# Kernel tuning notes

Hardware: AMD Instinct MI355X
Metric: run time of the kernel (lower is better)

Reference implementation:

```python
import jax, jax.numpy as jnp
import numpy as np

G, N = 1024, 40            # graphs, nodes per graph (complete graphs)
SLOPE = 0.1                # leaky relu negative slope
SMAT_IDX = jnp.array([0, 1, 2, 3, 1, 4, 5, 6, 2, 5, 7, 8, 3, 6, 8, 9])


def setup_inputs() -> dict:
    key = jax.random.key(0)
    ks = jax.random.split(key, 24)

    # --- graph structure: G identical complete graphs of N nodes ---
    ii, jj = np.meshgrid(np.arange(N), np.arange(N), indexing="ij")
    mask = ii != jj
    src_l, dst_l = ii[mask], jj[mask]              # directed edges per graph
    offs = (np.arange(G) * N)[:, None]
    edge_index = np.stack([(src_l[None] + offs).ravel(),
                           (dst_l[None] + offs).ravel()]).astype(np.int64)
    iu, ju = np.triu_indices(N, 1)
    M = iu.shape[0]                                 # 780 undirected edges
    ud_edges = np.stack([iu, ju], 1).astype(np.int64)
    edge_map = np.zeros((N, N), np.int64)
    edge_map[iu, ju] = np.arange(M)
    edge_map[ju, iu] = np.arange(M)

    def w(k, shape, fan_in):
        return jax.random.normal(k, shape, jnp.float32) / np.sqrt(fan_in)

    inp = {
        "x": jax.random.normal(ks[0], (G * N, 16), jnp.float32),
        "edge_index": jnp.asarray(edge_index),
        "ud_edges": jnp.asarray(ud_edges),
        "edge_map": jnp.asarray(edge_map),
        # GCN stack 6->32->32->64
        "Wg0": w(ks[1], (6, 32), 6),   "bg0": jnp.zeros((32,), jnp.float32),
        "Wg1": w(ks[2], (32, 32), 32), "bg1": jnp.zeros((32,), jnp.float32),
        "Wg2": w(ks[3], (32, 64), 32), "bg2": jnp.zeros((64,), jnp.float32),
        # node MLP 64->64->64->10
        "Wn0": w(ks[4], (64, 64), 64), "bn0": jnp.zeros((64,), jnp.float32),
        "Wn1": w(ks[5], (64, 64), 64), "bn1": jnp.zeros((64,), jnp.float32),
        "Wn2": w(ks[6], (64, 10), 64), "bn2": jnp.zeros((10,), jnp.float32),
        # edge MLP 64->64->64->10
        "We0": w(ks[7], (64, 64), 64), "be0": jnp.zeros((64,), jnp.float32),
        "We1": w(ks[8], (64, 64), 64), "be1": jnp.zeros((64,), jnp.float32),
        "We2": w(ks[9], (64, 10), 64), "be2": jnp.zeros((10,), jnp.float32),
    }
    return inp


def _forward(x, edge_index, ud_edges, edge_map,
             Wg0, bg0, Wg1, bg1, Wg2, bg2,
             Wn0, bn0, Wn1, bn1, Wn2, bn2,
             We0, be0, We1, be1, We2, be2):
    num_nodes = x.shape[0]
    h = x[:, :6]                                   # node_feature_mode == 1
    src, dst = edge_index[0], edge_index[1]

    # GCN normalization (add_self_loops=False, edge_weight=1)
    deg = jax.ops.segment_sum(jnp.ones(src.shape[0], x.dtype), dst,
                              num_segments=num_nodes)
    dis = jnp.where(deg > 0, jax.lax.rsqrt(jnp.maximum(deg, 1e-12)), 0.0)
    norm = dis[src] * dis[dst]                     # [E]

    def gcn(h, W, b):
        m = (h @ W)[src] * norm[:, None]
        return jax.ops.segment_sum(m, dst, num_segments=num_nodes) + b

    # eval mode: dropout is identity
    h = jax.nn.leaky_relu(gcn(h, Wg0, bg0), SLOPE)
    h = jax.nn.leaky_relu(gcn(h, Wg1, bg1), SLOPE)
    h = gcn(h, Wg2, bg2)                           # [G*N, 64]

    hg = h.reshape(G, N, -1)                       # [G, N, 64]

    def mlp(z, Ws, bs):
        for W, b in zip(Ws[:-1], bs[:-1]):
            z = jax.nn.leaky_relu(z @ W + b, SLOPE)
        return z @ Ws[-1] + bs[-1]

    vp = mlp(hg, [Wn0, Wn1, Wn2], [bn0, bn1, bn2])            # [G, N, 10]
    e = hg[:, ud_edges[:, 0], :] + hg[:, ud_edges[:, 1], :]   # [G, M, 64]
    ep = mlp(e, [We0, We1, We2], [be0, be1, be2])             # [G, M, 10]

    # recover_X: diag blocks smat(vp[i]), off-diag smat(ep[edge_map[i,j]])
    epm = ep[:, edge_map, :]                                  # [G, N, N, 10]
    eye = jnp.eye(N, dtype=bool)[None, :, :, None]
    vecs = jnp.where(eye, vp[:, :, None, :], epm)             # [G, N, N, 10]
    blocks = vecs[..., SMAT_IDX].reshape(G, N, N, 4, 4)
    X = blocks.transpose(0, 1, 3, 2, 4).reshape(G, 4 * N, 4 * N)
    return h, X


def reference(x, edge_index, ud_edges, edge_map,
              Wg0, bg0, Wg1, bg1, Wg2, bg2,
              Wn0, bn0, Wn1, bn1, Wn2, bn2,
              We0, be0, We1, be1, We2, be2):
    return _forward(x, edge_index, ud_edges, edge_map,
                    Wg0, bg0, Wg1, bg1, Wg2, bg2,
                    Wn0, bn0, Wn1, bn1, Wn2, bn2,
                    We0, be0, We1, be1, We2, be2)
```

## Files before the change

kernel.cpp:

```cpp
#include <hip/hip_runtime.h>

#define G_GRAPHS 1024
#define N_NODES  40
#define M_EDGES  780
#define NUM_NODES (G_GRAPHS * N_NODES)
#define H_ELEMS  (NUM_NODES * 64)
#define X_STRIDE 160
#define X_PER_G  25600
#define SLOPE 0.1f

#define EDGE_BLOCKS 6240
#define VP_BLOCKS   320
#define PACK_PER_MLP 9216

typedef __bf16 bf16x8 __attribute__((ext_vector_type(8)));
typedef unsigned short us8 __attribute__((ext_vector_type(8)));
typedef float f32x4 __attribute__((ext_vector_type(4)));

__device__ __forceinline__ float lrelu(float v) { return fmaxf(v, SLOPE * v); }
__device__ __forceinline__ unsigned short f2bf(float x) {
    __bf16 b = (__bf16)x;
    return __builtin_bit_cast(unsigned short, b);
}
__device__ __forceinline__ unsigned int pk2bf(float a, float b) {
    return (unsigned int)f2bf(a) | ((unsigned int)f2bf(b) << 16);
}

__global__ __launch_bounds__(256) void k_prep(const float* __restrict__ We0,
                                              const float* __restrict__ We1,
                                              const float* __restrict__ We2,
                                              const float* __restrict__ Wn0,
                                              const float* __restrict__ Wn1,
                                              const float* __restrict__ Wn2,
                                              unsigned short* __restrict__ wp) {
    int t = blockIdx.x * 256 + threadIdx.x;
    int mlp = t / PACK_PER_MLP;
    int o = t - mlp * PACK_PER_MLP;
    const float* W0 = mlp ? Wn0 : We0;
    const float* W1 = mlp ? Wn1 : We1;
    const float* W2 = mlp ? Wn2 : We2;
    float val;
    if (o < 8192) {
        const float* W = (o < 4096) ? W0 : W1;
        int idx = o & 4095;
        int j = idx & 7, l = (idx >> 3) & 63, tt = idx >> 9;
        int kt = tt & 1, mt = tt >> 1;
        int k = kt * 32 + ((l >> 4) & 3) * 8 + j;
        int m = mt * 16 + (l & 15);
        val = W[k * 64 + m];
    } else {
        int idx = o - 8192;
        int j = idx & 7, l = (idx >> 3) & 63, kt = idx >> 9;
        int k = kt * 32 + ((l >> 4) & 3) * 8 + j;
        int m = l & 15;
        val = (m < 10) ? W2[k * 10 + m] : 0.f;
    }
    wp[mlp * PACK_PER_MLP + o] = f2bf(val);
}

__global__ __launch_bounds__(256, 4) void k_gcn(const float* __restrict__ x,
                                                const float* __restrict__ Wg0,
                                                const float* __restrict__ bg0,
                                                const float* __restrict__ Wg1,
                                                const float* __restrict__ bg1,
                                                const float* __restrict__ Wg2,
                                                const float* __restrict__ bg2,
                                                float* __restrict__ hout) {
    __shared__ __align__(16) float h0[N_NODES * 6];
    __shared__ __align__(16) float buf[N_NODES * 64];
    __shared__ float S[64];
    __shared__ float P[8 * 64];
    __shared__ __align__(16) float h1[N_NODES * 32];
    __shared__ __align__(16) float h2[N_NODES * 32];

    const int g = blockIdx.x;
    const int tid = threadIdx.x;
    const float inv39 = 1.0f / 39.0f;
    const int c32 = tid & 31;
    const int c64 = tid & 63;

    float w0c[6], w1c[32], w2c[32];
#pragma unroll
    for (int f = 0; f < 6; f++)  w0c[f] = Wg0[f * 32 + c32];
#pragma unroll
    for (int m = 0; m < 32; m++) w1c[m] = Wg1[m * 32 + c32];
#pragma unroll
    for (int m = 0; m < 32; m++) w2c[m] = Wg2[m * 64 + c64];
    const float b0c = bg0[c32];
    const float b1c = bg1[c32];
    const float b2c = bg2[c64];

    for (int idx = tid; idx < N_NODES * 6; idx += 256) {
        int n = idx / 6, f = idx - n * 6;
        h0[idx] = x[(g * N_NODES + n) * 16 + f];
    }
    __syncthreads();

    {
        int n0 = tid >> 5;
#pragma unroll
        for (int t = 0; t < 5; t++) {
            int n = n0 + 8 * t;
            float s = 0.f;
#pragma unroll
            for (int f = 0; f < 6; f++) s += h0[n * 6 + f] * w0c[f];
            buf[n * 32 + c32] = s;
        }
    }
    __syncthreads();
    { int grp = tid >> 5; float s = 0.f;
#pragma unroll
      for (int n = grp * 5; n < grp * 5 + 5; n++) s += buf[n * 32 + c32];
      P[grp * 32 + c32] = s; }
    __syncthreads();
    if (tid < 32) { float s = 0.f;
#pragma unroll
      for (int grp = 0; grp < 8; grp++) s += P[grp * 32 + tid];
      S[tid] = s; }
    __syncthreads();
    for (int idx = tid; idx < N_NODES * 32; idx += 256)
        h1[idx] = lrelu((S[c32] - buf[idx]) * inv39 + b0c);
    __syncthreads();

    {
        int n0 = tid >> 5;
#pragma unroll
        for (int t = 0; t < 5; t++) {
            int n = n0 + 8 * t;
            const float4* hp = (const float4*)(h1 + n * 32);
            float s = 0.f;
#pragma unroll
            for (int q = 0; q < 8; q++) {
                float4 hv = hp[q];
                s += hv.x * w1c[4 * q + 0] + hv.y * w1c[4 * q + 1]
                   + hv.z * w1c[4 * q + 2] + hv.w * w1c[4 * q + 3];
            }
            buf[n * 32 + c32] = s;
        }
    }
    __syncthreads();
    { int grp = tid >> 5; float s = 0.f;
#pragma unroll
      for (int n = grp * 5; n < grp * 5 + 5; n++) s += buf[n * 32 + c32];
      P[grp * 32 + c32] = s; }
    __syncthreads();
    if (tid < 32) { float s = 0.f;
#pragma unroll
      for (int grp = 0; grp < 8; grp++) s += P[grp * 32 + tid];
      S[tid] = s; }
    __syncthreads();
    for (int idx = tid; idx < N_NODES * 32; idx += 256)
        h2[idx] = lrelu((S[c32] - buf[idx]) * inv39 + b1c);
    __syncthreads();

    {
        int n0 = tid >> 6;
#pragma unroll
        for (int t = 0; t < 10; t++) {
            int n = n0 + 4 * t;
            const float4* hp = (const float4*)(h2 + n * 32);
            float s = 0.f;
#pragma unroll
            for (int q = 0; q < 8; q++) {
                float4 hv = hp[q];
                s += hv.x * w2c[4 * q + 0] + hv.y * w2c[4 * q + 1]
                   + hv.z * w2c[4 * q + 2] + hv.w * w2c[4 * q + 3];
            }
            buf[n * 64 + c64] = s;
        }
    }
    __syncthreads();
    { int grp = tid >> 6; float s = 0.f;
#pragma unroll
      for (int n = grp * 10; n < grp * 10 + 10; n++) s += buf[n * 64 + c64];
      P[grp * 64 + c64] = s; }
    __syncthreads();
    if (tid < 64) { float s = 0.f;
#pragma unroll
      for (int grp = 0; grp < 4; grp++) s += P[grp * 64 + tid];
      S[tid] = s; }
    __syncthreads();
    for (int idx = tid; idx < N_NODES * 64; idx += 256)
        hout[g * N_NODES * 64 + idx] = (S[c64] - buf[idx]) * inv39 + b2c;
}

__global__ __launch_bounds__(256) void k_mlp(const float* __restrict__ h,
                                             const unsigned short* __restrict__ wp,
                                             const float* __restrict__ be0,
                                             const float* __restrict__ be1,
                                             const float* __restrict__ be2,
                                             const float* __restrict__ bn0,
                                             const float* __restrict__ bn1,
                                             const float* __restrict__ bn2,
                                             float* __restrict__ X) {
    __shared__ __align__(16) unsigned short sB[128 * 64];

    const int tid = threadIdx.x;
    const int l = tid & 63;
    const int w = tid >> 6;
    const int bid = blockIdx.x;
    const bool is_edge = (bid < EDGE_BLOCKS);

    const unsigned short* wb = wp + (is_edge ? 0 : PACK_PER_MLP);
    const float* b0 = is_edge ? be0 : bn0;
    const float* b1 = is_edge ? be1 : bn1;
    const float* b2 = is_edge ? be2 : bn2;

    const int r = 32 * w + (l >> 1);
    const int hf = l & 1;
    int g, i = 0, j = 0;
    if (is_edge) {
        int eid = bid * 128 + r;
        g = eid / M_EDGES;
        int m = eid - g * M_EDGES;
        float t = 6241.0f - 8.0f * (float)m;
        int i0 = (int)(0.5f * (79.0f - sqrtf(t)));
        i0 = min(38, max(0, i0));
        int cum = 39 * i0 - ((i0 * (i0 - 1)) >> 1);
        if (cum > m) { --i0; cum = 39 * i0 - ((i0 * (i0 - 1)) >> 1); }
        else if (m - cum >= 39 - i0) { cum += 39 - i0; ++i0; }
        i = i0;
        j = i0 + 1 + (m - cum);
    } else {
        int nid = (bid - EDGE_BLOCKS) * 128 + r;
        g = nid / N_NODES;
        i = nid - g * N_NODES;
        j = i;
    }

    {
        const float4* pa = (const float4*)(h + (g * N_NODES + i) * 64 + hf * 32);
        const float4* pb = (const float4*)(h + (g * N_NODES + j) * 64 + hf * 32);
        unsigned short tmp[32];
#pragma unroll
        for (int q = 0; q < 8; q++) {
            float4 a = pa[q];
            if (is_edge) {
                float4 b = pb[q];
                a.x += b.x; a.y += b.y; a.z += b.z; a.w += b.w;
            }
            tmp[4 * q + 0] = f2bf(a.x); tmp[4 * q + 1] = f2bf(a.y);
            tmp[4 * q + 2] = f2bf(a.z); tmp[4 * q + 3] = f2bf(a.w);
        }
#pragma unroll
        for (int q = 0; q < 4; q++) {
            int cs = (hf * 4 + q) ^ (r & 7);
            *(us8*)((char*)sB + r * 128 + cs * 16) = *(const us8*)(tmp + 8 * q);
        }
    }

    const int nl = l & 15;
    const int rq = (l >> 4) & 3;

    auto WA = [&](const unsigned short* base, int mt, int kt) -> bf16x8 {
        return __builtin_bit_cast(bf16x8,
            *(const us8*)(base + ((mt * 2 + kt) * 64 + l) * 8));
    };
    auto ZB = [&](const unsigned short* s, int nt, int kt) -> bf16x8 {
        int node = 32 * w + nt * 16 + nl;
        int cs = (kt * 4 + rq) ^ (node & 7);
        return __builtin_bit_cast(bf16x8,
            *(const us8*)((const char*)s + node * 128 + cs * 16));
    };
    auto zstore = [&](unsigned short* s, int mt, int nt, const f32x4& v) {
        int node = 32 * w + nt * 16 + nl;
        int cs = (mt * 2 + (rq >> 1)) ^ (node & 7);
        uint2 u = make_uint2(pk2bf(v[0], v[1]), pk2bf(v[2], v[3]));
        *(uint2*)((char*)s + node * 128 + cs * 16 + (rq & 1) * 8) = u;
    };

    {
        bf16x8 B[2][2];
#pragma unroll
        for (int nt = 0; nt < 2; nt++)
#pragma unroll
            for (int kt = 0; kt < 2; kt++) B[nt][kt] = ZB(sB, nt, kt);
#pragma unroll
        for (int mt = 0; mt < 4; mt++) {
            bf16x8 A0 = WA(wb, mt, 0), A1 = WA(wb, mt, 1);
            float4 bv = *(const float4*)(b0 + mt * 16 + rq * 4);
#pragma unroll
            for (int nt = 0; nt < 2; nt++) {
                f32x4 acc = (f32x4){0.f, 0.f, 0.f, 0.f};
                acc = __builtin_amdgcn_mfma_f32_16x16x32_bf16(A0, B[nt][0], acc, 0, 0, 0);
                acc = __builtin_amdgcn_mfma_f32_16x16x32_bf16(A1, B[nt][1], acc, 0, 0, 0);
                f32x4 z;
                z[0] = lrelu(acc[0] + bv.x); z[1] = lrelu(acc[1] + bv.y);
                z[2] = lrelu(acc[2] + bv.z); z[3] = lrelu(acc[3] + bv.w);
                zstore(sB, mt, nt, z);
            }
        }
    }

    {
        bf16x8 B[2][2];
#pragma unroll
        for (int nt = 0; nt < 2; nt++)
#pragma unroll
            for (int kt = 0; kt < 2; kt++) B[nt][kt] = ZB(sB, nt, kt);
        const unsigned short* w1p = wb + 4096;
#pragma unroll
        for (int mt = 0; mt < 4; mt++) {
            bf16x8 A0 = WA(w1p, mt, 0), A1 = WA(w1p, mt, 1);
            float4 bv = *(const float4*)(b1 + mt * 16 + rq * 4);
#pragma unroll
            for (int nt = 0; nt < 2; nt++) {
                f32x4 acc = (f32x4){0.f, 0.f, 0.f, 0.f};
                acc = __builtin_amdgcn_mfma_f32_16x16x32_bf16(A0, B[nt][0], acc, 0, 0, 0);
                acc = __builtin_amdgcn_mfma_f32_16x16x32_bf16(A1, B[nt][1], acc, 0, 0, 0);
                f32x4 z;
                z[0] = lrelu(acc[0] + bv.x); z[1] = lrelu(acc[1] + bv.y);
                z[2] = lrelu(acc[2] + bv.z); z[3] = lrelu(acc[3] + bv.w);
                zstore(sB, mt, nt, z);
            }
        }
    }

    float* sEPf = (float*)sB + w * 1024;
    {
        bf16x8 B[2][2];
#pragma unroll
        for (int nt = 0; nt < 2; nt++)
#pragma unroll
            for (int kt = 0; kt < 2; kt++) B[nt][kt] = ZB(sB, nt, kt);
        const unsigned short* w2p = wb + 8192;
        bf16x8 A0 = WA(w2p, 0, 0), A1 = WA(w2p, 0, 1);
        float bz[4];
#pragma unroll
        for (int k = 0; k < 4; k++) {
            int f = rq * 4 + k;
            bz[k] = (f < 10) ? b2[f] : 0.f;
        }
#pragma unroll
        for (int nt = 0; nt < 2; nt++) {
            f32x4 acc = (f32x4){0.f, 0.f, 0.f, 0.f};
            acc = __builtin_amdgcn_mfma_f32_16x16x32_bf16(A0, B[nt][0], acc, 0, 0, 0);
            acc = __builtin_amdgcn_mfma_f32_16x16x32_bf16(A1, B[nt][1], acc, 0, 0, 0);
            int nl2 = nt * 16 + nl;
            float4 v = make_float4(acc[0] + bz[0], acc[1] + bz[1],
                                   acc[2] + bz[2], acc[3] + bz[3]);
            *(float4*)(sEPf + nl2 * 20 + rq * 4) = v;
        }
    }

    {
        const float* ep = sEPf + (r & 31) * 20;
        float4 e0 = *(const float4*)(ep + 0);
        float4 e1 = *(const float4*)(ep + 4);
        float4 e2 = *(const float4*)(ep + 8);
        float4 r0 = make_float4(e0.x, e0.y, e0.z, e0.w);
        float4 r1 = make_float4(e0.y, e1.x, e1.y, e1.z);
        float4 r2 = make_float4(e0.z, e1.y, e1.w, e2.x);
        float4 r3 = make_float4(e0.w, e1.z, e2.x, e2.y);
        float* Xg = X + g * X_PER_G;
        if (is_edge) {
            int bi = hf ? j : i, bj = hf ? i : j;
            float* p = Xg + (4 * bi) * X_STRIDE + 4 * bj;
            *(float4*)(p + 0 * X_STRIDE) = r0;
            *(float4*)(p + 1 * X_STRIDE) = r1;
            *(float4*)(p + 2 * X_STRIDE) = r2;
            *(float4*)(p + 3 * X_STRIDE) = r3;
        } else {
            float* p = Xg + (4 * i + hf * 2) * X_STRIDE + 4 * i;
            if (hf == 0) {
                *(float4*)(p + 0 * X_STRIDE) = r0;
                *(float4*)(p + 1 * X_STRIDE) = r1;
            } else {
                *(float4*)(p + 0 * X_STRIDE) = r2;
                *(float4*)(p + 1 * X_STRIDE) = r3;
            }
        }
    }
}

extern "C" void kernel_launch(void* const* d_in, const int* in_sizes, int n_in,
                              void* d_out, int out_size, void* d_ws, size_t ws_size,
                              hipStream_t stream) {
    const float* x   = (const float*)d_in[0];
    const float* Wg0 = (const float*)d_in[4];
    const float* bg0 = (const float*)d_in[5];
    const float* Wg1 = (const float*)d_in[6];
    const float* bg1 = (const float*)d_in[7];
    const float* Wg2 = (const float*)d_in[8];
    const float* bg2 = (const float*)d_in[9];
    const float* Wn0 = (const float*)d_in[10];
    const float* bn0 = (const float*)d_in[11];
    const float* Wn1 = (const float*)d_in[12];
    const float* bn1 = (const float*)d_in[13];
    const float* Wn2 = (const float*)d_in[14];
    const float* bn2 = (const float*)d_in[15];
    const float* We0 = (const float*)d_in[16];
    const float* be0 = (const float*)d_in[17];
    const float* We1 = (const float*)d_in[18];
    const float* be1 = (const float*)d_in[19];
    const float* We2 = (const float*)d_in[20];
    const float* be2 = (const float*)d_in[21];

    float* hout = (float*)d_out;
    float* X    = hout + H_ELEMS;
    unsigned short* wp = (unsigned short*)d_ws;

    k_prep<<<72, 256, 0, stream>>>(We0, We1, We2, Wn0, Wn1, Wn2, wp);
    k_gcn<<<G_GRAPHS, 256, 0, stream>>>(x, Wg0, bg0, Wg1, bg1, Wg2, bg2, hout);
    k_mlp<<<EDGE_BLOCKS + VP_BLOCKS, 256, 0, stream>>>(hout, wp,
                                                       be0, be1, be2,
                                                       bn0, bn1, bn2, X);
}
```

Before: 231.3 us.

## Process one graph per block in MLP kernel with shared h and register weights

The MLP kernel now launches one block per graph instead of many edge/node blocks. It stages the graph's 40x64 node features in swizzled shared memory, keeps edge MLP weights resident in registers across chunks, and runs 27 32-row chunks (edges plus nodes) per block. X is then written cooperatively from a shared ep buffer. This cuts repeated global reads of h and weight reloads per block, at the cost of larger shared memory (~45KB), higher register pressure and only 1024 blocks.

```diff
diff --git a/kernel.cpp b/kernel.cpp
--- a/kernel.cpp
+++ b/kernel.cpp
@@ -9,8 +9,6 @@
 #define X_PER_G  25600
 #define SLOPE 0.1f
 
-#define EDGE_BLOCKS 6240
-#define VP_BLOCKS   320
 #define PACK_PER_MLP 9216
 
 typedef __bf16 bf16x8 __attribute__((ext_vector_type(8)));
@@ -184,6 +182,141 @@
         hout[g * N_NODES * 64 + idx] = (S[c64] - buf[idx]) * inv39 + b2c;
 }
 
+struct ChunkRegs {
+    bf16x8 A1[4][2];
+    bf16x8 A2[4][2];
+    bf16x8 A3[2];
+    float4 bv0[4];
+    float4 bv1[4];
+    float  bz[4];
+};
+
+__device__ __forceinline__ void run_chunk(int R0, int w, int l,
+                                          const float4* sh4,
+                                          unsigned short* sB,
+                                          float* sEP,
+                                          const ChunkRegs& cr) {
+    const int nl = l & 15;
+    const int rq = (l >> 4) & 3;
+
+    {
+        int rl = l >> 1, hf2 = l & 1;
+        int row = R0 + rl;
+        int ii = 0, jj = 0;
+        bool addf = false;
+        if (row < 780) {
+            float tq = 6241.0f - 8.0f * (float)row;
+            int i0 = (int)(0.5f * (79.0f - sqrtf(tq)));
+            i0 = min(38, max(0, i0));
+            int cum = 39 * i0 - ((i0 * (i0 - 1)) >> 1);
+            if (cum > row) { --i0; cum = 39 * i0 - ((i0 * (i0 - 1)) >> 1); }
+            else if (row - cum >= 39 - i0) { cum += 39 - i0; ++i0; }
+            ii = i0; jj = i0 + 1 + (row - cum);
+            addf = true;
+        } else if (row >= 800 && row < 840) {
+            ii = jj = row - 800;
+        }
+        unsigned short tmp[32];
+#pragma unroll
+        for (int q = 0; q < 8; q++) {
+            int u = hf2 * 8 + q;
+            float4 a = sh4[ii * 16 + (u ^ ((ii & 7) << 1))];
+            if (addf) {
+                float4 bq = sh4[jj * 16 + (u ^ ((jj & 7) << 1))];
+                a.x += bq.x; a.y += bq.y; a.z += bq.z; a.w += bq.w;
+            }
+            tmp[4 * q + 0] = f2bf(a.x); tmp[4 * q + 1] = f2bf(a.y);
+            tmp[4 * q + 2] = f2bf(a.z); tmp[4 * q + 3] = f2bf(a.w);
+        }
+        int r_sb = 32 * w + rl;
+#pragma unroll
+        for (int q = 0; q < 4; q++) {
+            int cs = (hf2 * 4 + q) ^ (r_sb & 7);
+            *(us8*)((char*)sB + r_sb * 128 + cs * 16) = *(const us8*)(tmp + 8 * q);
+        }
+    }
+
+    auto ZB = [&](int nt, int kt) -> bf16x8 {
+        int node = 32 * w + nt * 16 + nl;
+        int cs = (kt * 4 + rq) ^ (node & 7);
+        return __builtin_bit_cast(bf16x8,
+            *(const us8*)((const char*)sB + node * 128 + cs * 16));
+    };
+    auto zstore = [&](int mt, int nt, const f32x4& v) {
+        int node = 32 * w + nt * 16 + nl;
+        int cs = (mt * 2 + (rq >> 1)) ^ (node & 7);
+        uint2 u = make_uint2(pk2bf(v[0], v[1]), pk2bf(v[2], v[3]));
+        *(uint2*)((char*)sB + node * 128 + cs * 16 + (rq & 1) * 8) = u;
+    };
+
+    {
+        bf16x8 B[2][2];
+#pragma unroll
+        for (int nt = 0; nt < 2; nt++)
+#pragma unroll
+            for (int kt = 0; kt < 2; kt++) B[nt][kt] = ZB(nt, kt);
+#pragma unroll
+        for (int mt = 0; mt < 4; mt++) {
+            float4 bv = cr.bv0[mt];
+#pragma unroll
+            for (int nt = 0; nt < 2; nt++) {
+                f32x4 acc = (f32x4){0.f, 0.f, 0.f, 0.f};
+                acc = __builtin_amdgcn_mfma_f32_16x16x32_bf16(cr.A1[mt][0], B[nt][0], acc, 0, 0, 0);
+                acc = __builtin_amdgcn_mfma_f32_16x16x32_bf16(cr.A1[mt][1], B[nt][1], acc, 0, 0, 0);
+                f32x4 z;
+                z[0] = lrelu(acc[0] + bv.x); z[1] = lrelu(acc[1] + bv.y);
+                z[2] = lrelu(acc[2] + bv.z); z[3] = lrelu(acc[3] + bv.w);
+                zstore(mt, nt, z);
+            }
+        }
+    }
+
+    {
+        bf16x8 B[2][2];
+#pragma unroll
+        for (int nt = 0; nt < 2; nt++)
+#pragma unroll
+            for (int kt = 0; kt < 2; kt++) B[nt][kt] = ZB(nt, kt);
+#pragma unroll
+        for (int mt = 0; mt < 4; mt++) {
+            float4 bv = cr.bv1[mt];
+#pragma unroll
+            for (int nt = 0; nt < 2; nt++) {
+                f32x4 acc = (f32x4){0.f, 0.f, 0.f, 0.f};
+                acc = __builtin_amdgcn_mfma_f32_16x16x32_bf16(cr.A2[mt][0], B[nt][0], acc, 0, 0, 0);
+                acc = __builtin_amdgcn_mfma_f32_16x16x32_bf16(cr.A2[mt][1], B[nt][1], acc, 0, 0, 0);
+                f32x4 z;
+                z[0] = lrelu(acc[0] + bv.x); z[1] = lrelu(acc[1] + bv.y);
+                z[2] = lrelu(acc[2] + bv.z); z[3] = lrelu(acc[3] + bv.w);
+                zstore(mt, nt, z);
+            }
+        }
+    }
+
+    {
+        bf16x8 B[2][2];
+#pragma unroll
+        for (int nt = 0; nt < 2; nt++)
+#pragma unroll
+            for (int kt = 0; kt < 2; kt++) B[nt][kt] = ZB(nt, kt);
+#pragma unroll
+        for (int nt = 0; nt < 2; nt++) {
+            f32x4 acc = (f32x4){0.f, 0.f, 0.f, 0.f};
+            acc = __builtin_amdgcn_mfma_f32_16x16x32_bf16(cr.A3[0], B[nt][0], acc, 0, 0, 0);
+            acc = __builtin_amdgcn_mfma_f32_16x16x32_bf16(cr.A3[1], B[nt][1], acc, 0, 0, 0);
+            int rowe = R0 + nt * 16 + nl;
+            bool valid = (rowe < 780) || (rowe >= 800 && rowe < 840);
+            if (valid && rq < 3) {
+                int epr = (rowe < 780) ? rowe : rowe - 20;
+                float* p = sEP + epr * 10 + rq * 4;
+                *(float2*)p = make_float2(acc[0] + cr.bz[0], acc[1] + cr.bz[1]);
+                if (rq < 2)
+                    *(float2*)(p + 2) = make_float2(acc[2] + cr.bz[2], acc[3] + cr.bz[3]);
+            }
+        }
+    }
+}
+
 __global__ __launch_bounds__(256) void k_mlp(const float* __restrict__ h,
                                              const unsigned short* __restrict__ wp,
                                              const float* __restrict__ be0,
@@ -193,182 +326,117 @@
                                              const float* __restrict__ bn1,
                                              const float* __restrict__ bn2,
                                              float* __restrict__ X) {
+    __shared__ __align__(16) float sh[N_NODES * 64];
     __shared__ __align__(16) unsigned short sB[128 * 64];
+    __shared__ __align__(8)  float sEP[820 * 10];
 
     const int tid = threadIdx.x;
     const int l = tid & 63;
     const int w = tid >> 6;
-    const int bid = blockIdx.x;
-    const bool is_edge = (bid < EDGE_BLOCKS);
-
-    const unsigned short* wb = wp + (is_edge ? 0 : PACK_PER_MLP);
-    const float* b0 = is_edge ? be0 : bn0;
-    const float* b1 = is_edge ? be1 : bn1;
-    const float* b2 = is_edge ? be2 : bn2;
-
-    const int r = 32 * w + (l >> 1);
-    const int hf = l & 1;
-    int g, i = 0, j = 0;
-    if (is_edge) {
-        int eid = bid * 128 + r;
-        g = eid / M_EDGES;
-        int m = eid - g * M_EDGES;
-        float t = 6241.0f - 8.0f * (float)m;
-        int i0 = (int)(0.5f * (79.0f - sqrtf(t)));
-        i0 = min(38, max(0, i0));
-        int cum = 39 * i0 - ((i0 * (i0 - 1)) >> 1);
-        if (cum > m) { --i0; cum = 39 * i0 - ((i0 * (i0 - 1)) >> 1); }
-        else if (m - cum >= 39 - i0) { cum += 39 - i0; ++i0; }
-        i = i0;
-        j = i0 + 1 + (m - cum);
-    } else {
-        int nid = (bid - EDGE_BLOCKS) * 128 + r;
-        g = nid / N_NODES;
-        i = nid - g * N_NODES;
-        j = i;
-    }
-
-    {
-        const float4* pa = (const float4*)(h + (g * N_NODES + i) * 64 + hf * 32);
-        const float4* pb = (const float4*)(h + (g * N_NODES + j) * 64 + hf * 32);
-        unsigned short tmp[32];
-#pragma unroll
-        for (int q = 0; q < 8; q++) {
-            float4 a = pa[q];
-            if (is_edge) {
-                float4 b = pb[q];
-                a.x += b.x; a.y += b.y; a.z += b.z; a.w += b.w;
-            }
-            tmp[4 * q + 0] = f2bf(a.x); tmp[4 * q + 1] = f2bf(a.y);
-            tmp[4 * q + 2] = f2bf(a.z); tmp[4 * q + 3] = f2bf(a.w);
-        }
-#pragma unroll
-        for (int q = 0; q < 4; q++) {
-            int cs = (hf * 4 + q) ^ (r & 7);
-            *(us8*)((char*)sB + r * 128 + cs * 16) = *(const us8*)(tmp + 8 * q);
-        }
-    }
-
-    const int nl = l & 15;
+    const int g = blockIdx.x;
     const int rq = (l >> 4) & 3;
+
+    float4* sh4 = (float4*)sh;
+
+    {
+        const float4* hg4 = (const float4*)(h + g * (N_NODES * 64));
+#pragma unroll
+        for (int k = 0; k < 3; k++) {
+            int v = k * 256 + tid;
+            if (v < 640) {
+                int i = v >> 4, u = v & 15;
+                sh4[i * 16 + (u ^ ((i & 7) << 1))] = hg4[v];
+            }
+        }
+    }
 
     auto WA = [&](const unsigned short* base, int mt, int kt) -> bf16x8 {
         return __builtin_bit_cast(bf16x8,
             *(const us8*)(base + ((mt * 2 + kt) * 64 + l) * 8));
     };
-    auto ZB = [&](const unsigned short* s, int nt, int kt) -> bf16x8 {
-        int node = 32 * w + nt * 16 + nl;
-        int cs = (kt * 4 + rq) ^ (node & 7);
-        return __builtin_bit_cast(bf16x8,
-            *(const us8*)((const char*)s + node * 128 + cs * 16));
-    };
-    auto zstore = [&](unsigned short* s, int mt, int nt, const f32x4& v) {
-        int node = 32 * w + nt * 16 + nl;
-        int cs = (mt * 2 + (rq >> 1)) ^ (node & 7);
-        uint2 u = make_uint2(pk2bf(v[0], v[1]), pk2bf(v[2], v[3]));
-        *(uint2*)((char*)s + node * 128 + cs * 16 + (rq & 1) * 8) = u;
-    };
-
-    {
-        bf16x8 B[2][2];
-#pragma unroll
-        for (int nt = 0; nt < 2; nt++)
-#pragma unroll
-            for (int kt = 0; kt < 2; kt++) B[nt][kt] = ZB(sB, nt, kt);
-#pragma unroll
-        for (int mt = 0; mt < 4; mt++) {
-            bf16x8 A0 = WA(wb, mt, 0), A1 = WA(wb, mt, 1);
-            float4 bv = *(const float4*)(b0 + mt * 16 + rq * 4);
-#pragma unroll
-            for (int nt = 0; nt < 2; nt++) {
-                f32x4 acc = (f32x4){0.f, 0.f, 0.f, 0.f};
-                acc = __builtin_amdgcn_mfma_f32_16x16x32_bf16(A0, B[nt][0], acc, 0, 0, 0);
-                acc = __builtin_amdgcn_mfma_f32_16x16x32_bf16(A1, B[nt][1], acc, 0, 0, 0);
-                f32x4 z;
-                z[0] = lrelu(acc[0] + bv.x); z[1] = lrelu(acc[1] + bv.y);
-                z[2] = lrelu(acc[2] + bv.z); z[3] = lrelu(acc[3] + bv.w);
-                zstore(sB, mt, nt, z);
-            }
-        }
-    }
-
-    {
-        bf16x8 B[2][2];
-#pragma unroll
-        for (int nt = 0; nt < 2; nt++)
-#pragma unroll
-            for (int kt = 0; kt < 2; kt++) B[nt][kt] = ZB(sB, nt, kt);
-        const unsigned short* w1p = wb + 4096;
-#pragma unroll
-        for (int mt = 0; mt < 4; mt++) {
-            bf16x8 A0 = WA(w1p, mt, 0), A1 = WA(w1p, mt, 1);
-            float4 bv = *(const float4*)(b1 + mt * 16 + rq * 4);
-#pragma unroll
-            for (int nt = 0; nt < 2; nt++) {
-                f32x4 acc = (f32x4){0.f, 0.f, 0.f, 0.f};
-                acc = __builtin_amdgcn_mfma_f32_16x16x32_bf16(A0, B[nt][0], acc, 0, 0, 0);
-                acc = __builtin_amdgcn_mfma_f32_16x16x32_bf16(A1, B[nt][1], acc, 0, 0, 0);
-                f32x4 z;
-                z[0] = lrelu(acc[0] + bv.x); z[1] = lrelu(acc[1] + bv.y);
-                z[2] = lrelu(acc[2] + bv.z); z[3] = lrelu(acc[3] + bv.w);
-                zstore(sB, mt, nt, z);
-            }
-        }
-    }
-
-    float* sEPf = (float*)sB + w * 1024;
-    {
-        bf16x8 B[2][2];
-#pragma unroll
-        for (int nt = 0; nt < 2; nt++)
-#pragma unroll
-            for (int kt = 0; kt < 2; kt++) B[nt][kt] = ZB(sB, nt, kt);
-        const unsigned short* w2p = wb + 8192;
-        bf16x8 A0 = WA(w2p, 0, 0), A1 = WA(w2p, 0, 1);
-        float bz[4];
-#pragma unroll
-        for (int k = 0; k < 4; k++) {
-            int f = rq * 4 + k;
-            bz[k] = (f < 10) ? b2[f] : 0.f;
-        }
-#pragma unroll
-        for (int nt = 0; nt < 2; nt++) {
-            f32x4 acc = (f32x4){0.f, 0.f, 0.f, 0.f};
-            acc = __builtin_amdgcn_mfma_f32_16x16x32_bf16(A0, B[nt][0], acc, 0, 0, 0);
-            acc = __builtin_amdgcn_mfma_f32_16x16x32_bf16(A1, B[nt][1], acc, 0, 0, 0);
-            int nl2 = nt * 16 + nl;
-            float4 v = make_float4(acc[0] + bz[0], acc[1] + bz[1],
-                                   acc[2] + bz[2], acc[3] + bz[3]);
-            *(float4*)(sEPf + nl2 * 20 + rq * 4) = v;
-        }
-    }
-
-    {
-        const float* ep = sEPf + (r & 31) * 20;
-        float4 e0 = *(const float4*)(ep + 0);
-        float4 e1 = *(const float4*)(ep + 4);
-        float4 e2 = *(const float4*)(ep + 8);
-        float4 r0 = make_float4(e0.x, e0.y, e0.z, e0.w);
-        float4 r1 = make_float4(e0.y, e1.x, e1.y, e1.z);
-        float4 r2 = make_float4(e0.z, e1.y, e1.w, e2.x);
-        float4 r3 = make_float4(e0.w, e1.z, e2.x, e2.y);
-        float* Xg = X + g * X_PER_G;
-        if (is_edge) {
-            int bi = hf ? j : i, bj = hf ? i : j;
+
+    ChunkRegs ce;
+#pragma unroll
+    for (int mt = 0; mt < 4; mt++) {
+#pragma unroll
+        for (int kt = 0; kt < 2; kt++) {
+            ce.A1[mt][kt] = WA(wp, mt, kt);
+            ce.A2[mt][kt] = WA(wp + 4096, mt, kt);
+        }
+        ce.bv0[mt] = *(const float4*)(be0 + mt * 16 + rq * 4);
+        ce.bv1[mt] = *(const float4*)(be1 + mt * 16 + rq * 4);
+    }
+    ce.A3[0] = WA(wp + 8192, 0, 0);
+    ce.A3[1] = WA(wp + 8192, 0, 1);
+#pragma unroll
+    for (int k = 0; k < 4; k++) {
+        int f = rq * 4 + k;
+        ce.bz[k] = (f < 10) ? be2[f] : 0.f;
+    }
+
+    __syncthreads();
+
+    for (int c = w; c < 27; c += 4) {
+        if (c < 25) {
+            run_chunk(c * 32, w, l, sh4, sB, sEP, ce);
+        } else {
+            const unsigned short* wn = wp + PACK_PER_MLP;
+            ChunkRegs cn;
+#pragma unroll
+            for (int mt = 0; mt < 4; mt++) {
+#pragma unroll
+                for (int kt = 0; kt < 2; kt++) {
+                    cn.A1[mt][kt] = WA(wn, mt, kt);
+                    cn.A2[mt][kt] = WA(wn + 4096, mt, kt);
+                }
+                cn.bv0[mt] = *(const float4*)(bn0 + mt * 16 + rq * 4);
+                cn.bv1[mt] = *(const float4*)(bn1 + mt * 16 + rq * 4);
+            }
+            cn.A3[0] = WA(wn + 8192, 0, 0);
+            cn.A3[1] = WA(wn + 8192, 0, 1);
+#pragma unroll
+            for (int k = 0; k < 4; k++) {
+                int f = rq * 4 + k;
+                cn.bz[k] = (f < 10) ? bn2[f] : 0.f;
+            }
+            run_chunk(c * 32, w, l, sh4, sB, sEP, cn);
+        }
+    }
+
+    __syncthreads();
+
+    float* Xg = X + g * X_PER_G;
+#pragma unroll
+    for (int k = 0; k < 7; k++) {
+        int b = k * 256 + tid;
+        if (b < 1600) {
+            int bi = b / 40;
+            int bj = b - bi * 40;
+            int ridx;
+            if (bi == bj) {
+                ridx = 780 + bi;
+            } else {
+                int mn = min(bi, bj), mx = max(bi, bj);
+                ridx = 39 * mn - ((mn * (mn - 1)) >> 1) + (mx - mn - 1);
+            }
+            const float* ep = sEP + ridx * 10;
+            float2 e0 = *(const float2*)(ep + 0);
+            float2 e1 = *(const float2*)(ep + 2);
+            float2 e2 = *(const float2*)(ep + 4);
+            float2 e3 = *(const float2*)(ep + 6);
+            float2 e4 = *(const float2*)(ep + 8);
+            float f0 = e0.x, f1 = e0.y, f2 = e1.x, f3 = e1.y;
+            float f4 = e2.x, f5 = e2.y, f6 = e3.x, f7 = e3.y;
+            float f8 = e4.x, f9 = e4.y;
+            float4 r0 = make_float4(f0, f1, f2, f3);
+            float4 r1 = make_float4(f1, f4, f5, f6);
+            float4 r2 = make_float4(f2, f5, f7, f8);
+            float4 r3 = make_float4(f3, f6, f8, f9);
             float* p = Xg + (4 * bi) * X_STRIDE + 4 * bj;
             *(float4*)(p + 0 * X_STRIDE) = r0;
             *(float4*)(p + 1 * X_STRIDE) = r1;
             *(float4*)(p + 2 * X_STRIDE) = r2;
             *(float4*)(p + 3 * X_STRIDE) = r3;
-        } else {
-            float* p = Xg + (4 * i + hf * 2) * X_STRIDE + 4 * i;
-            if (hf == 0) {
-                *(float4*)(p + 0 * X_STRIDE) = r0;
-                *(float4*)(p + 1 * X_STRIDE) = r1;
-            } else {
-                *(float4*)(p + 0 * X_STRIDE) = r2;
-                *(float4*)(p + 1 * X_STRIDE) = r3;
-            }
         }
     }
 }
@@ -402,7 +470,7 @@
 
     k_prep<<<72, 256, 0, stream>>>(We0, We1, We2, Wn0, Wn1, Wn2, wp);
     k_gcn<<<G_GRAPHS, 256, 0, stream>>>(x, Wg0, bg0, Wg1, bg1, Wg2, bg2, hout);
-    k_mlp<<<EDGE_BLOCKS + VP_BLOCKS, 256, 0, stream>>>(hout, wp,
-                                                       be0, be1, be2,
-                                                       bn0, bn1, bn2, X);
-}
+    k_mlp<<<G_GRAPHS, 256, 0, stream>>>(hout, wp,
+                                        be0, be1, be2,
+                                        bn0, bn1, bn2, X);
+}
```

Result: no change. 233.0 us (+0.7%).
